# Kernel tuning notes

Hardware: AMD Instinct MI355X
Metric: run time of the kernel (lower is better)

Reference implementation:

```python
import jax, jax.numpy as jnp
import numpy as np

B, T, E, D = 8, 2048, 1024, 64  # batch, seq_len, n_emb, head_dim

def setup_inputs() -> dict:
    key = jax.random.key(0)
    ks = jax.random.split(key, 4)
    scale = 1.0 / np.sqrt(E)
    return {
        "x": jax.random.normal(ks[0], (B, T, E), dtype=jnp.float32),
        "Wq": jax.random.normal(ks[1], (E, D), dtype=jnp.float32) * scale,
        "bq": jnp.zeros((D,), dtype=jnp.float32),
        "Wk": jax.random.normal(ks[2], (E, D), dtype=jnp.float32) * scale,
        "bk": jnp.zeros((D,), dtype=jnp.float32),
        "Wv": jax.random.normal(ks[3], (E, D), dtype=jnp.float32) * scale,
        "bv": jnp.zeros((D,), dtype=jnp.float32),
    }

def reference(x, Wq, bq, Wk, bk, Wv, bv):
    # QKV projections: [B,T,E] @ [E,D] -> [B,T,D]
    q = x @ Wq + bq
    k = x @ Wk + bk
    v = x @ Wv + bv
    d = q.shape[-1]
    # scaled dot-product scores [B,T,T]
    wei = jnp.einsum('btd,bsd->bts', q, k) * (d ** -0.5)
    # causal mask: position t attends to s <= t
    t = wei.shape[1]
    causal = jnp.tril(jnp.ones((t, t), dtype=bool))
    wei = jnp.where(causal, wei, -jnp.inf)
    wei = jax.nn.softmax(wei, axis=-1)
    # attention output [B,T,D]
    return jnp.einsum('bts,bsd->btd', wei, v)
```

## Files before the change

kernel.cpp:

```cpp
#include <hip/hip_runtime.h>
#include <math.h>


#define B_   8
#define T_   2048
#define E_   1024
#define D_   64
#define BT_  (B_ * T_)

typedef __attribute__((ext_vector_type(8))) short s16x8;
typedef __attribute__((ext_vector_type(4))) short s16x4;
typedef __attribute__((ext_vector_type(4))) float f32x4;

__device__ __forceinline__ short f2bf(float f) {
    union { float f; unsigned u; } a; a.f = f;
    unsigned r = a.u + 0x7fffu + ((a.u >> 16) & 1u);
    return (short)(r >> 16);
}

#define MFMA16(a, b, c) __builtin_amdgcn_mfma_f32_16x16x32_bf16((a), (b), (c), 0, 0, 0)

#define DPPF(x, ctrl) __builtin_bit_cast(float, \
    __builtin_amdgcn_update_dpp(0, __builtin_bit_cast(int, (x)), (ctrl), 0xF, 0xF, true))

__device__ __forceinline__ float rsum16(float x) {
    x += DPPF(x, 0xB1);
    x += DPPF(x, 0x4E);
    x += DPPF(x, 0x124);
    x += DPPF(x, 0x128);
    return x;
}

__global__ __launch_bounds__(256) void wtrans_kernel(
    const float* __restrict__ Wq, const float* __restrict__ Wk,
    const float* __restrict__ Wv, short* __restrict__ Wt)
{
    __shared__ float sT[64][65];
    const int sel = blockIdx.x >> 4;
    const int k0  = (blockIdx.x & 15) * 64;
    const float* W = sel == 0 ? Wq : (sel == 1 ? Wk : Wv);
    const int t  = threadIdx.x;
    const int kr = t >> 4, c4 = (t & 15) * 4;
    #pragma unroll
    for (int i = 0; i < 4; ++i) {
        float4 v = *(const float4*)&W[(size_t)(k0 + kr + i * 16) * D_ + c4];
        sT[kr + i * 16][c4 + 0] = v.x; sT[kr + i * 16][c4 + 1] = v.y;
        sT[kr + i * 16][c4 + 2] = v.z; sT[kr + i * 16][c4 + 3] = v.w;
    }
    __syncthreads();
    #pragma unroll
    for (int i = 0; i < 4; ++i) {
        int n  = (t >> 4) + i * 16;
        int kk = (t & 15) * 4;
        s16x4 o;
        o.x = f2bf(sT[kk + 0][n]); o.y = f2bf(sT[kk + 1][n]);
        o.z = f2bf(sT[kk + 2][n]); o.w = f2bf(sT[kk + 3][n]);
        *(s16x4*)&Wt[(size_t)(sel * 64 + n) * E_ + k0 + kk] = o;
    }
}

__global__ __launch_bounds__(512) void qkv_kernel(
    const float* __restrict__ x, const short* __restrict__ Wt,
    const float* __restrict__ bq, const float* __restrict__ bk,
    const float* __restrict__ bv,
    short* __restrict__ Qg, short* __restrict__ Kg, short* __restrict__ VTg)
{
    __shared__ short sX[2][64 * 140];
    const int tid  = threadIdx.x;
    const int lane = tid & 63;
    const int w    = tid >> 6;
    const int l15  = lane & 15, quad = lane >> 4;
    const int h2   = w & 1;
    const int n2   = w >> 1;
    const int t0   = blockIdx.x * 64;
    const int bb   = t0 >> 11;

    const int srow = tid >> 3;
    const int skc  = (tid & 7) * 16;
    const float* px = &x[(size_t)(t0 + srow) * E_ + skc];

    f32x4 acc[3][2];
    #pragma unroll
    for (int a = 0; a < 3; ++a)
        #pragma unroll
        for (int h = 0; h < 2; ++h)
            acc[a][h] = (f32x4){0.f, 0.f, 0.f, 0.f};

    float4 lda0 = *(const float4*)(px +   0);
    float4 lda1 = *(const float4*)(px +   4);
    float4 lda2 = *(const float4*)(px +   8);
    float4 lda3 = *(const float4*)(px +  12);
    float4 ldb0 = *(const float4*)(px + 128);
    float4 ldb1 = *(const float4*)(px + 132);
    float4 ldb2 = *(const float4*)(px + 136);
    float4 ldb3 = *(const float4*)(px + 140);

    int buf = 0;
    for (int k0 = 0; k0 < E_; k0 += 128) {
        s16x8 pk0, pk1;
        pk0[0] = f2bf(lda0.x); pk0[1] = f2bf(lda0.y);
        pk0[2] = f2bf(lda0.z); pk0[3] = f2bf(lda0.w);
        pk0[4] = f2bf(lda1.x); pk0[5] = f2bf(lda1.y);
        pk0[6] = f2bf(lda1.z); pk0[7] = f2bf(lda1.w);
        pk1[0] = f2bf(lda2.x); pk1[1] = f2bf(lda2.y);
        pk1[2] = f2bf(lda2.z); pk1[3] = f2bf(lda2.w);
        pk1[4] = f2bf(lda3.x); pk1[5] = f2bf(lda3.y);
        pk1[6] = f2bf(lda3.z); pk1[7] = f2bf(lda3.w);
        *(s16x8*)&sX[buf][srow * 140 + skc]     = pk0;
        *(s16x8*)&sX[buf][srow * 140 + skc + 8] = pk1;
        __syncthreads();

        lda0 = ldb0; lda1 = ldb1; lda2 = ldb2; lda3 = ldb3;
        if (k0 + 256 < E_) {
            const float* p2 = px + k0 + 256;
            ldb0 = *(const float4*)(p2 +  0);
            ldb1 = *(const float4*)(p2 +  4);
            ldb2 = *(const float4*)(p2 +  8);
            ldb3 = *(const float4*)(p2 + 12);
        }

        s16x8 aw[3][4];
        #pragma unroll
        for (int t3 = 0; t3 < 3; ++t3) {
            const short* pw = &Wt[(size_t)((n2 * 3 + t3) * 16 + l15) * E_ + k0 + quad * 8];
            #pragma unroll
            for (int kc = 0; kc < 4; ++kc)
                aw[t3][kc] = *(const s16x8*)(pw + kc * 32);
        }
        s16x8 bxf[2][4];
        #pragma unroll
        for (int h = 0; h < 2; ++h) {
            const int trow = (h2 * 2 + h) * 16 + l15;
            #pragma unroll
            for (int kc = 0; kc < 4; ++kc)
                bxf[h][kc] = *(const s16x8*)&sX[buf][trow * 140 + kc * 32 + quad * 8];
        }
        #pragma unroll
        for (int t3 = 0; t3 < 3; ++t3)
            #pragma unroll
            for (int h = 0; h < 2; ++h)
                #pragma unroll
                for (int kc = 0; kc < 4; ++kc)
                    acc[t3][h] = MFMA16(aw[t3][kc], bxf[h][kc], acc[t3][h]);
        buf ^= 1;
    }

    __syncthreads();
    short* sVT = &sX[0][0];

    #pragma unroll
    for (int t3 = 0; t3 < 3; ++t3) {
        const int nt = n2 * 3 + t3;
        const int fb = (nt & 3) * 16 + quad * 4;
        const float* bias = nt < 4 ? bq : (nt < 8 ? bk : bv);
        f32x4 bsv = *(const f32x4*)&bias[fb];
        #pragma unroll
        for (int h = 0; h < 2; ++h) {
            const int lt  = (h2 * 2 + h) * 16 + l15;
            const int tok = t0 + lt;
            f32x4 v = acc[t3][h] + bsv;
            if (nt < 4) {
                v *= 0.125f;
                s16x4 o = { f2bf(v[0]), f2bf(v[1]), f2bf(v[2]), f2bf(v[3]) };
                *(s16x4*)&Qg[(size_t)tok * D_ + fb] = o;
            } else if (nt < 8) {
                s16x4 o = { f2bf(v[0]), f2bf(v[1]), f2bf(v[2]), f2bf(v[3]) };
                *(s16x4*)&Kg[(size_t)tok * D_ + fb] = o;
            } else {
                #pragma unroll
                for (int r = 0; r < 4; ++r)
                    sVT[(fb + r) * 72 + lt] = f2bf(v[r]);
            }
        }
    }
    __syncthreads();
    {
        const int d  = tid >> 3;
        const int tq = (tid & 7) * 8;
        s16x8 vv = *(const s16x8*)&sVT[d * 72 + tq];
        *(s16x8*)&VTg[(size_t)(bb * D_ + d) * T_ + (t0 & (T_ - 1)) + tq] = vv;
    }
}

__global__ __launch_bounds__(512) void attn_kernel(
    const short* __restrict__ Qg, const short* __restrict__ Kg,
    const short* __restrict__ VTg, float* __restrict__ out)
{
    __shared__ char smem[74752];
    short* sP = (short*)smem;
    float* sO = (float*)smem;
    float* sl = (float*)(smem + 73728);

    const int tid  = threadIdx.x;
    const int lane = tid & 63;
    const int w    = tid >> 6;
    const int l15  = lane & 15, quad = lane >> 4;
    const int b    = blockIdx.x & 7;
    const int j    = blockIdx.x >> 3;
    const int tq   = j * 32;
    const int nch  = (j >> 1) + 1;
    const int c0   = (w * nch) >> 3;
    const int c1   = ((w + 1) * nch) >> 3;

    s16x8 aq[2][2];
    #pragma unroll
    for (int qt = 0; qt < 2; ++qt) {
        const size_t qoff = ((size_t)b * T_ + tq + qt * 16 + l15) * D_ + quad * 8;
        aq[qt][0] = *(const s16x8*)&Qg[qoff];
        aq[qt][1] = *(const s16x8*)&Qg[qoff + 32];
    }

    f32x4 oo[2][4];
    float lp[2][4];
    #pragma unroll
    for (int qt = 0; qt < 2; ++qt) {
        #pragma unroll
        for (int nt = 0; nt < 4; ++nt)
            oo[qt][nt] = (f32x4){0.f, 0.f, 0.f, 0.f};
        #pragma unroll
        for (int r = 0; r < 4; ++r) lp[qt][r] = 0.f;
    }

    const short* kb = Kg  + (size_t)b * T_ * D_;
    const short* vb = VTg + (size_t)b * D_ * T_;
    short* sPw = sP + w * (2 * 16 * 72);

    for (int cc = c0; cc < c1; ++cc) {
        const int s0 = cc * 64;
        s16x8 bk[4][2];
        #pragma unroll
        for (int nt = 0; nt < 4; ++nt) {
            const short* pk = kb + (size_t)(s0 + nt * 16 + l15) * D_ + quad * 8;
            bk[nt][0] = *(const s16x8*)pk;
            bk[nt][1] = *(const s16x8*)(pk + 32);
        }
        const f32x4 zz = (f32x4){0.f, 0.f, 0.f, 0.f};
        f32x4 sacc[2][4];
        #pragma unroll
        for (int qt = 0; qt < 2; ++qt)
            #pragma unroll
            for (int nt = 0; nt < 4; ++nt) {
                sacc[qt][nt] = MFMA16(aq[qt][0], bk[nt][0], zz);
                sacc[qt][nt] = MFMA16(aq[qt][1], bk[nt][1], sacc[qt][nt]);
            }
        s16x8 bv[4][2];
        #pragma unroll
        for (int nt = 0; nt < 4; ++nt) {
            const short* pv = vb + (size_t)(nt * 16 + l15) * T_ + s0 + quad * 8;
            bv[nt][0] = *(const s16x8*)pv;
            bv[nt][1] = *(const s16x8*)(pv + 32);
        }
        const bool diag = (cc == nch - 1);
        float p[2][4][4];
        #pragma unroll
        for (int qt = 0; qt < 2; ++qt)
            #pragma unroll
            for (int nt = 0; nt < 4; ++nt)
                #pragma unroll
                for (int r = 0; r < 4; ++r) {
                    float e = __expf(sacc[qt][nt][r]);
                    if (diag && (s0 + nt * 16 + l15 > tq + qt * 16 + quad * 4 + r))
                        e = 0.f;
                    p[qt][nt][r] = e;
                }
        #pragma unroll
        for (int qt = 0; qt < 2; ++qt)
            #pragma unroll
            for (int r = 0; r < 4; ++r)
                lp[qt][r] += (p[qt][0][r] + p[qt][1][r]) + (p[qt][2][r] + p[qt][3][r]);
        #pragma unroll
        for (int qt = 0; qt < 2; ++qt)
            #pragma unroll
            for (int nt = 0; nt < 4; ++nt)
                #pragma unroll
                for (int r = 0; r < 4; ++r)
                    sPw[qt * (16 * 72) + (quad * 4 + r) * 72 + nt * 16 + l15] =
                        f2bf(p[qt][nt][r]);
        #pragma unroll
        for (int qt = 0; qt < 2; ++qt) {
            s16x8 ap0 = *(const s16x8*)&sPw[qt * (16 * 72) + l15 * 72 + quad * 8];
            s16x8 ap1 = *(const s16x8*)&sPw[qt * (16 * 72) + l15 * 72 + 32 + quad * 8];
            #pragma unroll
            for (int nt = 0; nt < 4; ++nt) {
                oo[qt][nt] = MFMA16(ap0, bv[nt][0], oo[qt][nt]);
                oo[qt][nt] = MFMA16(ap1, bv[nt][1], oo[qt][nt]);
            }
        }
    }

    f32x4 lv[2];
    #pragma unroll
    for (int qt = 0; qt < 2; ++qt)
        #pragma unroll
        for (int r = 0; r < 4; ++r)
            lv[qt][r] = rsum16(lp[qt][r]);

    __syncthreads();
    {
        float* sOw = sO + w * (64 * 36);
        #pragma unroll
        for (int qt = 0; qt < 2; ++qt)
            #pragma unroll
            for (int nt = 0; nt < 4; ++nt)
                *(f32x4*)&sOw[(nt * 16 + l15) * 36 + qt * 16 + quad * 4] = oo[qt][nt];
        if (l15 == 0) {
            *(f32x4*)&sl[w * 32 + quad * 4]      = lv[0];
            *(f32x4*)&sl[w * 32 + 16 + quad * 4] = lv[1];
        }
    }
    __syncthreads();
    {
        const int d  = tid & 63;
        const int rb = (tid >> 6) * 4;
        f32x4 osum = (f32x4){0.f, 0.f, 0.f, 0.f};
        f32x4 lsum = (f32x4){0.f, 0.f, 0.f, 0.f};
        #pragma unroll
        for (int w2 = 0; w2 < 8; ++w2) {
            osum += *(const f32x4*)&sO[w2 * (64 * 36) + d * 36 + rb];
            lsum += *(const f32x4*)&sl[w2 * 32 + rb];
        }
        #pragma unroll
        for (int i = 0; i < 4; ++i)
            out[((size_t)b * T_ + tq + rb + i) * D_ + d] = osum[i] / lsum[i];
    }
}

extern "C" void kernel_launch(void* const* d_in, const int* in_sizes, int n_in,
                              void* d_out, int out_size, void* d_ws, size_t ws_size,
                              hipStream_t stream) {
    (void)in_sizes; (void)n_in; (void)out_size; (void)ws_size;
    const float* x  = (const float*)d_in[0];
    const float* Wq = (const float*)d_in[1];
    const float* bq = (const float*)d_in[2];
    const float* Wk = (const float*)d_in[3];
    const float* bk = (const float*)d_in[4];
    const float* Wv = (const float*)d_in[5];
    const float* bv = (const float*)d_in[6];

    char* ws = (char*)d_ws;
    short* Qg  = (short*)(ws);
    short* Kg  = (short*)(ws + (size_t)2 * 1024 * 1024);
    short* VTg = (short*)(ws + (size_t)4 * 1024 * 1024);
    short* Wt  = (short*)(ws + (size_t)6 * 1024 * 1024);

    wtrans_kernel<<<48, 256, 0, stream>>>(Wq, Wk, Wv, Wt);
    qkv_kernel<<<BT_ / 64, 512, 0, stream>>>(x, Wt, bq, bk, bv, Qg, Kg, VTg);
    attn_kernel<<<B_ * 64, 512, 0, stream>>>(Qg, Kg, VTg, (float*)d_out);
}
```

Measured before the change: 151.7 us.

## Stream x tiles directly to LDS with global_load_lds and convert at read

Replaces the register-staged load, bf16 conversion and LDS store of x tiles in the QKV projection with direct global-to-LDS async loads of fp32 data into a double buffer. Conversion to bf16 now happens when each wave reads its MFMA operands from LDS. This is meant to cut VGPR pressure and the per-iteration store path. In exchange it doubles LDS footprint (fp32, unpadded rows, which risks bank conflicts) and repeats the conversion work on every read of a row.

```diff
diff --git a/kernel.cpp b/kernel.cpp
--- a/kernel.cpp
+++ b/kernel.cpp
@@ -19,6 +19,12 @@
 }
 
 #define MFMA16(a, b, c) __builtin_amdgcn_mfma_f32_16x16x32_bf16((a), (b), (c), 0, 0, 0)
+
+typedef __attribute__((address_space(1))) const unsigned int gu32;
+typedef __attribute__((address_space(3)))       unsigned int su32;
+__device__ __forceinline__ void gld16(const void* g, void* s) {
+    __builtin_amdgcn_global_load_lds((gu32*)g, (su32*)s, 16, 0, 0);
+}
 
 #define DPPF(x, ctrl) __builtin_bit_cast(float, \
     __builtin_amdgcn_update_dpp(0, __builtin_bit_cast(int, (x)), (ctrl), 0xF, 0xF, true))
@@ -65,7 +71,7 @@
     const float* __restrict__ bv,
     short* __restrict__ Qg, short* __restrict__ Kg, short* __restrict__ VTg)
 {
-    __shared__ short sX[2][64 * 140];
+    __shared__ char sXm[2 * 64 * 128 * 4];
     const int tid  = threadIdx.x;
     const int lane = tid & 63;
     const int w    = tid >> 6;
@@ -75,9 +81,8 @@
     const int t0   = blockIdx.x * 64;
     const int bb   = t0 >> 11;
 
-    const int srow = tid >> 3;
-    const int skc  = (tid & 7) * 16;
-    const float* px = &x[(size_t)(t0 + srow) * E_ + skc];
+    const int grow = lane >> 5;
+    const int gcol = (lane & 31) << 2;
 
     f32x4 acc[3][2];
     #pragma unroll
@@ -86,39 +91,16 @@
         for (int h = 0; h < 2; ++h)
             acc[a][h] = (f32x4){0.f, 0.f, 0.f, 0.f};
 
-    float4 lda0 = *(const float4*)(px +   0);
-    float4 lda1 = *(const float4*)(px +   4);
-    float4 lda2 = *(const float4*)(px +   8);
-    float4 lda3 = *(const float4*)(px +  12);
-    float4 ldb0 = *(const float4*)(px + 128);
-    float4 ldb1 = *(const float4*)(px + 132);
-    float4 ldb2 = *(const float4*)(px + 136);
-    float4 ldb3 = *(const float4*)(px + 140);
+    #pragma unroll
+    for (int j = 0; j < 4; ++j) {
+        const int cc  = (w << 2) + j;
+        const int row = (cc << 1) + grow;
+        gld16(&x[(size_t)(t0 + row) * E_ + gcol], sXm + cc * 1024);
+    }
+    __syncthreads();
 
     int buf = 0;
     for (int k0 = 0; k0 < E_; k0 += 128) {
-        s16x8 pk0, pk1;
-        pk0[0] = f2bf(lda0.x); pk0[1] = f2bf(lda0.y);
-        pk0[2] = f2bf(lda0.z); pk0[3] = f2bf(lda0.w);
-        pk0[4] = f2bf(lda1.x); pk0[5] = f2bf(lda1.y);
-        pk0[6] = f2bf(lda1.z); pk0[7] = f2bf(lda1.w);
-        pk1[0] = f2bf(lda2.x); pk1[1] = f2bf(lda2.y);
-        pk1[2] = f2bf(lda2.z); pk1[3] = f2bf(lda2.w);
-        pk1[4] = f2bf(lda3.x); pk1[5] = f2bf(lda3.y);
-        pk1[6] = f2bf(lda3.z); pk1[7] = f2bf(lda3.w);
-        *(s16x8*)&sX[buf][srow * 140 + skc]     = pk0;
-        *(s16x8*)&sX[buf][srow * 140 + skc + 8] = pk1;
-        __syncthreads();
-
-        lda0 = ldb0; lda1 = ldb1; lda2 = ldb2; lda3 = ldb3;
-        if (k0 + 256 < E_) {
-            const float* p2 = px + k0 + 256;
-            ldb0 = *(const float4*)(p2 +  0);
-            ldb1 = *(const float4*)(p2 +  4);
-            ldb2 = *(const float4*)(p2 +  8);
-            ldb3 = *(const float4*)(p2 + 12);
-        }
-
         s16x8 aw[3][4];
         #pragma unroll
         for (int t3 = 0; t3 < 3; ++t3) {
@@ -127,13 +109,32 @@
             for (int kc = 0; kc < 4; ++kc)
                 aw[t3][kc] = *(const s16x8*)(pw + kc * 32);
         }
+        if (k0 + 128 < E_) {
+            const char* dst = sXm + (buf ^ 1) * 32768;
+            #pragma unroll
+            for (int j = 0; j < 4; ++j) {
+                const int cc  = (w << 2) + j;
+                const int row = (cc << 1) + grow;
+                gld16(&x[(size_t)(t0 + row) * E_ + k0 + 128 + gcol],
+                      (void*)(dst + cc * 1024));
+            }
+        }
         s16x8 bxf[2][4];
         #pragma unroll
         for (int h = 0; h < 2; ++h) {
             const int trow = (h2 * 2 + h) * 16 + l15;
-            #pragma unroll
-            for (int kc = 0; kc < 4; ++kc)
-                bxf[h][kc] = *(const s16x8*)&sX[buf][trow * 140 + kc * 32 + quad * 8];
+            const char* rb = sXm + buf * 32768 + trow * 512 + quad * 32;
+            #pragma unroll
+            for (int kc = 0; kc < 4; ++kc) {
+                float4 xa = *(const float4*)(rb + kc * 128);
+                float4 xb = *(const float4*)(rb + kc * 128 + 16);
+                s16x8 f;
+                f[0] = f2bf(xa.x); f[1] = f2bf(xa.y);
+                f[2] = f2bf(xa.z); f[3] = f2bf(xa.w);
+                f[4] = f2bf(xb.x); f[5] = f2bf(xb.y);
+                f[6] = f2bf(xb.z); f[7] = f2bf(xb.w);
+                bxf[h][kc] = f;
+            }
         }
         #pragma unroll
         for (int t3 = 0; t3 < 3; ++t3)
@@ -142,11 +143,11 @@
                 #pragma unroll
                 for (int kc = 0; kc < 4; ++kc)
                     acc[t3][h] = MFMA16(aw[t3][kc], bxf[h][kc], acc[t3][h]);
+        __syncthreads();
         buf ^= 1;
     }
 
-    __syncthreads();
-    short* sVT = &sX[0][0];
+    short* sVT = (short*)sXm;
 
     #pragma unroll
     for (int t3 = 0; t3 < 3; ++t3) {
```

Measured after the change: 158.3 us. +4.4%, slower.
